# Optimization experiments

Measured on AMD Instinct MI355X. Metric: run time of the kernel, lower is better.

The kernel has to match this reference:

```python
import jax, jax.numpy as jnp
import numpy as np

# TT factorization: vocab = 8*8*8*8*16 = 65536, dim = 4^5 = 1024, rank 16
SHAPE = [(8, 4), (8, 4), (8, 4), (8, 4), (16, 4)]
RANKS = [1, 16, 16, 16, 16, 1]
VOCAB = 65536
DIM = 1024
BATCH, SEQ = 8, 2048


def setup_inputs() -> dict:
    key = jax.random.key(0)
    ks = jax.random.split(key, len(SHAPE) + 1)
    inp = {}
    for k, (n, m) in enumerate(SHAPE):
        core = jax.random.normal(ks[k], (RANKS[k], n * m, RANKS[k + 1]), dtype=jnp.float32) * 0.01
        inp[f"core{k}"] = core
    inp["indices"] = jax.random.randint(ks[-1], (BATCH, SEQ), 0, VOCAB)
    return inp


def _tt_full(cores):
    # Faithful port of tt_to_matrix: chain matmul of cores, then a flat reshape
    # to (VOCAB, DIM).  (The original code reshapes merged_shape -> (rows, cols)
    # directly, without the inverse interleave permute; we replicate that.)
    result = cores[0]  # (1, n0*m0, r1)
    for core in cores[1:]:
        r_prev = result.shape[-1]
        result = (result.reshape(-1, r_prev) @ core.reshape(r_prev, -1))
        result = result.reshape(1, -1, core.shape[-1])
    return result.reshape(VOCAB, DIM)


def reference(core0, core1, core2, core3, core4, indices):
    full = _tt_full([core0, core1, core2, core3, core4])  # (VOCAB, DIM)
    return jnp.take(full, indices, axis=0)              # (BATCH, SEQ, DIM)
```

## Files before the change

kernel.cpp:

```cpp
#include <hip/hip_runtime.h>
#include <hip/hip_bf16.h>


typedef float f32x4 __attribute__((ext_vector_type(4)));
typedef short bf16x8 __attribute__((ext_vector_type(8)));
typedef short s16x4 __attribute__((ext_vector_type(4)));
typedef unsigned int uint2v __attribute__((ext_vector_type(2)));

static __device__ __forceinline__ unsigned short f2bf(float x) {
    __hip_bfloat16 h = __float2bfloat16(x);
    return *reinterpret_cast<unsigned short*>(&h);
}

__global__ __launch_bounds__(256) void tt_mfrag(
    const float* __restrict__ c3,
    const float* __restrict__ c4,
    unsigned short* __restrict__ mfrag)
{
    const int tid  = blockIdx.x * 256 + threadIdx.x;
    const int tile = tid >> 9;
    const int lane = (tid >> 3) & 63;
    const int i    = tid & 7;
    const int k = 4 * (lane >> 4) + (i & 3) + ((i >> 2) << 4);
    const int d = (tile << 4) + (lane & 15);
    const int r3 = k & 15;
    const int b  = k >> 4;
    const int i3 = (b << 4) + (d >> 6);
    const int i4 = d & 63;
    float acc = 0.f;
    #pragma unroll
    for (int r4 = 0; r4 < 16; ++r4)
        acc = fmaf(c3[(r3 * 32 + i3) * 16 + r4], c4[(r4 << 6) + i4], acc);
    mfrag[tid] = f2bf(acc);
}

__global__ __launch_bounds__(256) void tt_fused_expand(
    const float* __restrict__ c0, const float* __restrict__ c1,
    const float* __restrict__ c2, const int* __restrict__ idx,
    const unsigned short* __restrict__ mfrag,
    float* __restrict__ out, int n_tokens)
{
    const int t  = threadIdx.x;
    const int tl = t >> 4;
    const int r  = t & 15;
    const int token = blockIdx.x * 16 + tl;
    const int v = (token < n_tokens) ? idx[token] : 0;

    __shared__ float w2b[16][20];
    __shared__ float w3b[16][20];
    __shared__ unsigned int w3e[16][18];

    {
        const int i0 = (v >> 11) & 31;
        const int i1 = (v >> 6) & 31;
        float w2r = 0.f;
        #pragma unroll
        for (int r1 = 0; r1 < 16; ++r1)
            w2r = fmaf(c0[i0 * 16 + r1], c1[(r1 * 32 + i1) * 16 + r], w2r);
        w2b[tl][r] = w2r;
    }
    float4 w2v[4];
    #pragma unroll
    for (int q = 0; q < 4; ++q)
        w2v[q] = *(const float4*)&w2b[tl][q << 2];

    {
        const int i2 = (v >> 1) & 31;
        float w3r = 0.f;
        #pragma unroll
        for (int q = 0; q < 4; ++q) {
            w3r = fmaf(w2v[q].x, c2[((q * 4 + 0) * 32 + i2) * 16 + r], w3r);
            w3r = fmaf(w2v[q].y, c2[((q * 4 + 1) * 32 + i2) * 16 + r], w3r);
            w3r = fmaf(w2v[q].z, c2[((q * 4 + 2) * 32 + i2) * 16 + r], w3r);
            w3r = fmaf(w2v[q].w, c2[((q * 4 + 3) * 32 + i2) * 16 + r], w3r);
        }
        w3b[tl][r] = w3r;
    }
    {
        const int vlow = v & 1;
        const int k0 = 2 * r, k1 = 2 * r + 1;
        const float f0 = w3b[tl][k0 & 15];
        const float f1 = w3b[tl][k1 & 15];
        const unsigned int lo = ((k0 >> 4) == vlow) ? f2bf(f0) : 0u;
        const unsigned int hi = ((k1 >> 4) == vlow) ? f2bf(f1) : 0u;
        w3e[tl][r] = lo | (hi << 16);
    }

    __syncthreads();

    {
        const int w   = t >> 6;
        const int l   = t & 63;
        const int col = l & 15;
        const int g   = l >> 4;

        const int tok = blockIdx.x * 16 + col;
        const bool ok = (tok < n_tokens);

        const uint2v ulo = *(const uint2v*)&w3e[col][2 * g];
        const uint2v uhi = *(const uint2v*)&w3e[col][8 + 2 * g];
        const s16x4 blo = *(const s16x4*)&ulo;
        const s16x4 bhi = *(const s16x4*)&uhi;
        const bf16x8 bf = {blo.x, blo.y, blo.z, blo.w,
                           bhi.x, bhi.y, bhi.z, bhi.w};

        float* outp = out + (size_t)tok * 1024 + (g << 2);

        #pragma unroll
        for (int n = 0; n < 16; ++n) {
            const int T = w * 16 + n;
            const bf16x8 af = *(const bf16x8*)(mfrag + (size_t)T * 512 + l * 8);
            f32x4 acc = {0.f, 0.f, 0.f, 0.f};
            acc = __builtin_amdgcn_mfma_f32_16x16x32_bf16(af, bf, acc, 0, 0, 0);
            if (ok)
                __builtin_nontemporal_store(acc, (f32x4*)(outp + (T << 4)));
        }
    }
}

#define RSTRIDE 20
#define GSTRIDE 328

__global__ __launch_bounds__(256) void tt_embed_fused(
    const float* __restrict__ c0, const float* __restrict__ c1,
    const float* __restrict__ c2, const float* __restrict__ c3,
    const float* __restrict__ c4, const int* __restrict__ idx,
    float* __restrict__ out, int n_tokens)
{
    const int t   = threadIdx.x;
    const int tl  = t >> 5;
    const int l32 = t & 31;
    const int r   = t & 15;
    const int l   = t & 63;
    const int wid = t >> 6;
    const int token = blockIdx.x * 8 + tl;
    const int v = (token < n_tokens) ? idx[token] : 0;

    __shared__ float w4s[8 * GSTRIDE];
    __shared__ float w2b[8][20];
    __shared__ float w3b[8][20];

    float4 c4v[16];
    #pragma unroll
    for (int r4 = 0; r4 < 16; ++r4)
        c4v[r4] = *(const float4*)(c4 + (r4 << 6) + ((l & 15) << 2));

    {
        const int i0 = (v >> 11) & 31, i1 = (v >> 6) & 31;
        float w2r = 0.f;
        #pragma unroll
        for (int r1 = 0; r1 < 16; ++r1)
            w2r = fmaf(c0[i0 * 16 + r1], c1[(r1 * 32 + i1) * 16 + r], w2r);
        w2b[tl][r] = w2r;
    }
    float4 w2v[4];
    #pragma unroll
    for (int q = 0; q < 4; ++q)
        w2v[q] = *(const float4*)&w2b[tl][q << 2];
    {
        const int i2 = (v >> 1) & 31;
        float w3r = 0.f;
        #pragma unroll
        for (int q = 0; q < 4; ++q) {
            w3r = fmaf(w2v[q].x, c2[((q * 4 + 0) * 32 + i2) * 16 + r], w3r);
            w3r = fmaf(w2v[q].y, c2[((q * 4 + 1) * 32 + i2) * 16 + r], w3r);
            w3r = fmaf(w2v[q].z, c2[((q * 4 + 2) * 32 + i2) * 16 + r], w3r);
            w3r = fmaf(w2v[q].w, c2[((q * 4 + 3) * 32 + i2) * 16 + r], w3r);
        }
        w3b[tl][r] = w3r;
    }
    float4 w3v[4];
    #pragma unroll
    for (int q = 0; q < 4; ++q)
        w3v[q] = *(const float4*)&w3b[tl][q << 2];
    {
        const int vlow16 = (v & 1) << 4;
        float4 a0 = {0,0,0,0}, a1 = {0,0,0,0};
        const float wv_arr0[16] = {w3v[0].x, w3v[0].y, w3v[0].z, w3v[0].w,
                                   w3v[1].x, w3v[1].y, w3v[1].z, w3v[1].w,
                                   w3v[2].x, w3v[2].y, w3v[2].z, w3v[2].w,
                                   w3v[3].x, w3v[3].y, w3v[3].z, w3v[3].w};
        #pragma unroll
        for (int r3 = 0; r3 < 16; ++r3) {
            const float wv = wv_arr0[r3];
            const float* base = c3 + ((r3 * 32 + vlow16) << 4);
            const float4 b0 = *(const float4*)(base + (l32 << 2));
            const float4 b1 = *(const float4*)(base + 128 + (l32 << 2));
            a0.x = fmaf(wv, b0.x, a0.x); a0.y = fmaf(wv, b0.y, a0.y);
            a0.z = fmaf(wv, b0.z, a0.z); a0.w = fmaf(wv, b0.w, a0.w);
            a1.x = fmaf(wv, b1.x, a1.x); a1.y = fmaf(wv, b1.y, a1.y);
            a1.z = fmaf(wv, b1.z, a1.z); a1.w = fmaf(wv, b1.w, a1.w);
        }
        float* sb = &w4s[tl * GSTRIDE + ((l32 & 3) << 2)];
        *(float4*)(sb + ((l32 >> 2)    ) * RSTRIDE) = a0;
        *(float4*)(sb + (8 + (l32 >> 2)) * RSTRIDE) = a1;
    }
    #pragma unroll
    for (int s = 0; s < 2; ++s) {
        const int slot = 2 * wid + s;
        const int tok  = blockIdx.x * 8 + slot;
        const float* slab = &w4s[slot * GSTRIDE];
        const int sub = l >> 4;
        const int colb = (l & 15) << 2;
        #pragma unroll
        for (int j = 0; j < 4; ++j) {
            const int row = (j << 2) + sub;
            const float* rp = slab + row * RSTRIDE;
            const float4 wa = *(const float4*)(rp);
            const float4 wb = *(const float4*)(rp + 4);
            const float4 wc = *(const float4*)(rp + 8);
            const float4 wd = *(const float4*)(rp + 12);
            float4 acc = {0,0,0,0};
            #define FB4(WV, K)                           \
                acc.x = fmaf(WV, c4v[K].x, acc.x);       \
                acc.y = fmaf(WV, c4v[K].y, acc.y);       \
                acc.z = fmaf(WV, c4v[K].z, acc.z);       \
                acc.w = fmaf(WV, c4v[K].w, acc.w);
            FB4(wa.x,  0) FB4(wa.y,  1) FB4(wa.z,  2) FB4(wa.w,  3)
            FB4(wb.x,  4) FB4(wb.y,  5) FB4(wb.z,  6) FB4(wb.w,  7)
            FB4(wc.x,  8) FB4(wc.y,  9) FB4(wc.z, 10) FB4(wc.w, 11)
            FB4(wd.x, 12) FB4(wd.y, 13) FB4(wd.z, 14) FB4(wd.w, 15)
            #undef FB4
            if (tok < n_tokens)
                __builtin_nontemporal_store(*(const f32x4*)&acc,
                    (f32x4*)(out + (size_t)tok * 1024 + (row << 6) + colb));
        }
    }
}

extern "C" void kernel_launch(void* const* d_in, const int* in_sizes, int n_in,
                              void* d_out, int out_size, void* d_ws, size_t ws_size,
                              hipStream_t stream) {
    const float* c0  = (const float*)d_in[0];
    const float* c1  = (const float*)d_in[1];
    const float* c2  = (const float*)d_in[2];
    const float* c3  = (const float*)d_in[3];
    const float* c4  = (const float*)d_in[4];
    const int*   idx = (const int*)d_in[5];
    float* out = (float*)d_out;

    const int n_tokens = in_sizes[5];
    const size_t ws_needed = 65536 + 256;

    if (ws_size >= ws_needed) {
        unsigned short* mfrag = (unsigned short*)d_ws;
        const int ngrp = (n_tokens + 15) / 16;
        tt_mfrag<<<128, 256, 0, stream>>>(c3, c4, mfrag);
        tt_fused_expand<<<ngrp, 256, 0, stream>>>(c0, c1, c2, idx, mfrag,
                                                  out, n_tokens);
    } else {
        const int grid = (n_tokens + 7) / 8;
        tt_embed_fused<<<grid, 256, 0, stream>>>(c0, c1, c2, c3, c4, idx, out,
                                                 n_tokens);
    }
}
```

Measured before the change: 30.09 us.

## Split per-token coefficient prep from MFMA expansion and register-cache mfrag tiles

The per-token TT chain (c0·c1·c2 contractions that produce bf16 B fragments) moves into a prep kernel, merged with the mfrag computation as extra blocks of one launch. The results go to workspace in fragment layout. A new lean expand kernel holds all 16 mfrag A-fragments per wave in registers, processes two token groups per block, and only does MFMA plus streaming stores. The aim is to make the store-bound expand kernel free of the scalar FMA chains and LDS syncs. The cost is a workspace round-trip for the fragments and a larger workspace requirement.

```diff
diff --git a/kernel.cpp b/kernel.cpp
--- a/kernel.cpp
+++ b/kernel.cpp
@@ -4,46 +4,45 @@
 
 typedef float f32x4 __attribute__((ext_vector_type(4)));
 typedef short bf16x8 __attribute__((ext_vector_type(8)));
-typedef short s16x4 __attribute__((ext_vector_type(4)));
-typedef unsigned int uint2v __attribute__((ext_vector_type(2)));
 
 static __device__ __forceinline__ unsigned short f2bf(float x) {
     __hip_bfloat16 h = __float2bfloat16(x);
     return *reinterpret_cast<unsigned short*>(&h);
 }
 
-__global__ __launch_bounds__(256) void tt_mfrag(
-    const float* __restrict__ c3,
-    const float* __restrict__ c4,
-    unsigned short* __restrict__ mfrag)
+__global__ __launch_bounds__(256) void tt_prep(
+    const float* __restrict__ c0, const float* __restrict__ c1,
+    const float* __restrict__ c2, const float* __restrict__ c3,
+    const float* __restrict__ c4, const int* __restrict__ idx,
+    unsigned short* __restrict__ mfrag,
+    unsigned char*  __restrict__ w3xf,
+    int n_tokens)
 {
-    const int tid  = blockIdx.x * 256 + threadIdx.x;
-    const int tile = tid >> 9;
-    const int lane = (tid >> 3) & 63;
-    const int i    = tid & 7;
-    const int k = 4 * (lane >> 4) + (i & 3) + ((i >> 2) << 4);
-    const int d = (tile << 4) + (lane & 15);
-    const int r3 = k & 15;
-    const int b  = k >> 4;
-    const int i3 = (b << 4) + (d >> 6);
-    const int i4 = d & 63;
-    float acc = 0.f;
-    #pragma unroll
-    for (int r4 = 0; r4 < 16; ++r4)
-        acc = fmaf(c3[(r3 * 32 + i3) * 16 + r4], c4[(r4 << 6) + i4], acc);
-    mfrag[tid] = f2bf(acc);
-}
-
-__global__ __launch_bounds__(256) void tt_fused_expand(
-    const float* __restrict__ c0, const float* __restrict__ c1,
-    const float* __restrict__ c2, const int* __restrict__ idx,
-    const unsigned short* __restrict__ mfrag,
-    float* __restrict__ out, int n_tokens)
-{
-    const int t  = threadIdx.x;
+    const int t = threadIdx.x;
+
+    if (blockIdx.x < 128) {
+        const int tid  = blockIdx.x * 256 + t;
+        const int tile = tid >> 9;
+        const int lane = (tid >> 3) & 63;
+        const int i    = tid & 7;
+        const int k = 4 * (lane >> 4) + (i & 3) + ((i >> 2) << 4);
+        const int d = (tile << 4) + (lane & 15);
+        const int r3 = k & 15;
+        const int b  = k >> 4;
+        const int i3 = (b << 4) + (d >> 6);
+        const int i4 = d & 63;
+        float acc = 0.f;
+        #pragma unroll
+        for (int r4 = 0; r4 < 16; ++r4)
+            acc = fmaf(c3[(r3 * 32 + i3) * 16 + r4], c4[(r4 << 6) + i4], acc);
+        mfrag[tid] = f2bf(acc);
+        return;
+    }
+
+    const int gb = blockIdx.x - 128;
     const int tl = t >> 4;
     const int r  = t & 15;
-    const int token = blockIdx.x * 16 + tl;
+    const int token = gb * 16 + tl;
     const int v = (token < n_tokens) ? idx[token] : 0;
 
     __shared__ float w2b[16][20];
@@ -79,41 +78,61 @@
     {
         const int vlow = v & 1;
         const int k0 = 2 * r, k1 = 2 * r + 1;
-        const float f0 = w3b[tl][k0 & 15];
-        const float f1 = w3b[tl][k1 & 15];
-        const unsigned int lo = ((k0 >> 4) == vlow) ? f2bf(f0) : 0u;
-        const unsigned int hi = ((k1 >> 4) == vlow) ? f2bf(f1) : 0u;
+        const unsigned int lo = ((k0 >> 4) == vlow) ? f2bf(w3b[tl][k0 & 15]) : 0u;
+        const unsigned int hi = ((k1 >> 4) == vlow) ? f2bf(w3b[tl][k1 & 15]) : 0u;
         w3e[tl][r] = lo | (hi << 16);
     }
 
     __syncthreads();
 
-    {
-        const int w   = t >> 6;
-        const int l   = t & 63;
-        const int col = l & 15;
-        const int g   = l >> 4;
-
-        const int tok = blockIdx.x * 16 + col;
+    if (t < 64) {
+        const int col = t & 15, g = t >> 4;
+        uint4 wf;
+        wf.x = w3e[col][2 * g];
+        wf.y = w3e[col][2 * g + 1];
+        wf.z = w3e[col][8 + 2 * g];
+        wf.w = w3e[col][8 + 2 * g + 1];
+        *(uint4*)(w3xf + (size_t)gb * 1024 + t * 16) = wf;
+    }
+}
+
+__global__ __launch_bounds__(256) void tt_expand(
+    const unsigned short* __restrict__ mfrag,
+    const unsigned char*  __restrict__ w3xf,
+    float* __restrict__ out, int n_tokens, int ngrp)
+{
+    const int t = threadIdx.x;
+    const int w = t >> 6;
+    const int l = t & 63;
+    const int col = l & 15;
+    const int g   = l >> 4;
+
+    bf16x8 mf[16];
+    #pragma unroll
+    for (int n = 0; n < 16; ++n)
+        mf[n] = *(const bf16x8*)(mfrag + (((w << 4) + n) << 9) + (l << 3));
+
+    const int g0 = blockIdx.x * 2;
+    const int g1c = (g0 + 1 < ngrp) ? (g0 + 1) : (ngrp - 1);
+
+    const bf16x8 bfa = *(const bf16x8*)(w3xf + (size_t)g0  * 1024 + l * 16);
+    const bf16x8 bfb = *(const bf16x8*)(w3xf + (size_t)g1c * 1024 + l * 16);
+
+    #pragma unroll
+    for (int s = 0; s < 2; ++s) {
+        const int grp = g0 + s;
+        if (grp >= ngrp) break;
+        const bf16x8 bf = s ? bfb : bfa;
+        const int tok = grp * 16 + col;
         const bool ok = (tok < n_tokens);
-
-        const uint2v ulo = *(const uint2v*)&w3e[col][2 * g];
-        const uint2v uhi = *(const uint2v*)&w3e[col][8 + 2 * g];
-        const s16x4 blo = *(const s16x4*)&ulo;
-        const s16x4 bhi = *(const s16x4*)&uhi;
-        const bf16x8 bf = {blo.x, blo.y, blo.z, blo.w,
-                           bhi.x, bhi.y, bhi.z, bhi.w};
-
-        float* outp = out + (size_t)tok * 1024 + (g << 2);
+        float* outp = out + (size_t)tok * 1024 + (w << 8) + (g << 2);
 
         #pragma unroll
         for (int n = 0; n < 16; ++n) {
-            const int T = w * 16 + n;
-            const bf16x8 af = *(const bf16x8*)(mfrag + (size_t)T * 512 + l * 8);
             f32x4 acc = {0.f, 0.f, 0.f, 0.f};
-            acc = __builtin_amdgcn_mfma_f32_16x16x32_bf16(af, bf, acc, 0, 0, 0);
+            acc = __builtin_amdgcn_mfma_f32_16x16x32_bf16(mf[n], bf, acc, 0, 0, 0);
             if (ok)
-                __builtin_nontemporal_store(acc, (f32x4*)(outp + (T << 4)));
+                __builtin_nontemporal_store(acc, (f32x4*)(outp + (n << 4)));
         }
     }
 }
@@ -240,14 +259,16 @@
     float* out = (float*)d_out;
 
     const int n_tokens = in_sizes[5];
-    const size_t ws_needed = 65536 + 256;
+    const int ngrp = (n_tokens + 15) / 16;
+    const size_t ws_needed = 65536 + (size_t)ngrp * 1024 + 256;
 
     if (ws_size >= ws_needed) {
         unsigned short* mfrag = (unsigned short*)d_ws;
-        const int ngrp = (n_tokens + 15) / 16;
-        tt_mfrag<<<128, 256, 0, stream>>>(c3, c4, mfrag);
-        tt_fused_expand<<<ngrp, 256, 0, stream>>>(c0, c1, c2, idx, mfrag,
-                                                  out, n_tokens);
+        unsigned char*  w3xf  = (unsigned char*)d_ws + 65536;
+        tt_prep<<<128 + ngrp, 256, 0, stream>>>(c0, c1, c2, c3, c4, idx,
+                                                mfrag, w3xf, n_tokens);
+        tt_expand<<<(ngrp + 1) / 2, 256, 0, stream>>>(mfrag, w3xf, out,
+                                                      n_tokens, ngrp);
     } else {
         const int grid = (n_tokens + 7) / 8;
         tt_embed_fused<<<grid, 256, 0, stream>>>(c0, c1, c2, c3, c4, idx, out,
```

After: 29.06 us. 3.4% less time.
